# Optimization experiments

Measured on AMD Instinct MI355X. Metric: run time of the kernel, lower is better.

The kernel has to match this reference:

```python
import jax, jax.numpy as jnp
import numpy as np

NQ = 6       # total qubits
NF = 4
NL = 2       # layers
B = 65536    # batch
WEIGHT_INIT_STD = 0.01


def _apply_1q(state, gate, w):
    """Apply a 2x2 gate (shared (2,2) or per-sample (B,2,2)) to qubit w.
    state: (B, 2,2,2,2,2,2) complex64, axis w+1 is qubit w (PennyLane wire order)."""
    ax = w + 1
    s = jnp.moveaxis(state, ax, -1)
    shp = s.shape
    s = s.reshape(shp[0], -1, 2)
    if gate.ndim == 2:
        s = jnp.einsum('ij,bkj->bki', gate, s)
    else:
        s = jnp.einsum('bij,bkj->bki', gate, s)
    return jnp.moveaxis(s.reshape(shp), -1, ax)


def _cnot(state, c, t):
    """CNOT with control c, target t: flip target axis where control bit = 1."""
    ac, at = c + 1, t + 1
    s0 = jax.lax.index_in_dim(state, 0, ac, keepdims=True)
    s1 = jnp.flip(jax.lax.index_in_dim(state, 1, ac, keepdims=True), axis=at)
    return jnp.concatenate([s0, s1], axis=ac)


def _ry(theta):
    ct = jnp.cos(theta * 0.5)
    st = jnp.sin(theta * 0.5)
    return jnp.stack([jnp.stack([ct, -st]), jnp.stack([st, ct])]).astype(jnp.complex64)


def _circuit(x, weights, ancilla_bias):
    b = x.shape[0]
    state = jnp.zeros((b,) + (2,) * NQ, jnp.complex64)
    state = state.at[(slice(None),) + (0,) * NQ].set(1.0)  # |000000>
    # RX(x[:, w]) encoding on qubits 0..3 (batched gates)
    half = x.astype(jnp.float32) * 0.5
    c = jnp.cos(half).astype(jnp.complex64)
    s = (-1j) * jnp.sin(half).astype(jnp.complex64)
    for w in range(NF):
        g = jnp.stack([jnp.stack([c[:, w], s[:, w]], -1),
                       jnp.stack([s[:, w], c[:, w]], -1)], -2)  # (B,2,2)
        state = _apply_1q(state, g, w)
    # RY ancilla init on qubits 4, 5
    state = _apply_1q(state, _ry(ancilla_bias[0]), 4)
    state = _apply_1q(state, _ry(ancilla_bias[1]), 5)
    # entangling layers: CNOT ring then RY rotations
    for l in range(weights.shape[0]):
        for w in range(NQ):
            state = _cnot(state, w, (w + 1) % NQ)
        for w in range(NQ):
            state = _apply_1q(state, _ry(weights[l, w]), w)
    # <Z_w> for w in 0..3
    p = state.real ** 2 + state.imag ** 2  # (B,2,...,2)
    outs = []
    for w in range(NF):
        pw = p.sum(axis=tuple(a for a in range(1, NQ + 1) if a != w + 1))  # (B,2)
        outs.append(pw[:, 0] - pw[:, 1])
    return jnp.stack(outs, -1).astype(jnp.float32)  # (B, 4)


def setup_inputs() -> dict:
    key = jax.random.key(0)
    k1, k2 = jax.random.split(key)
    x = jax.random.normal(k1, (B, NF), jnp.float32)
    weights = jax.random.normal(k2, (NL, NQ), jnp.float32) * WEIGHT_INIT_STD
    ancilla_bias = jnp.zeros((2,), jnp.float32)
    return {"x": x, "weights": weights, "ancilla_bias": ancilla_bias}


def reference(x, weights, ancilla_bias):
    return _circuit(x, weights, ancilla_bias)
```

## Files before the change

### kernel.cpp

```cpp
#include <hip/hip_runtime.h>


#define NL 2

typedef float v2f __attribute__((ext_vector_type(2)));

template<int CTRL>
__device__ __forceinline__ float dppf(float v) {
    return __int_as_float(__builtin_amdgcn_update_dpp(
        0, __float_as_int(v), CTRL, 0xF, 0xF, true));
}
template<int CTRL>
__device__ __forceinline__ v2f dpp2(v2f v) {
    v2f r; r.x = dppf<CTRL>(v.x); r.y = dppf<CTRL>(v.y); return r;
}
__device__ __forceinline__ v2f splat(float f) { v2f r; r.x = f; r.y = f; return r; }

#define QP_XOR1  0xB1
#define QP_XOR2  0x4E
#define QP_C45   0xB4
#define QP_BC0   0x00
#define QP_BC1   0x55
#define QP_BC2   0xAA
#define QP_BC3   0xFF

__global__ __launch_bounds__(256) void qcirc6_dpp_kernel(
    const float* __restrict__ x,
    const float* __restrict__ weights,
    const float* __restrict__ bias,
    float* __restrict__ out,
    int B)
{
    const int gid = blockIdx.x * blockDim.x + threadIdx.x;
    const int sample = gid >> 2;
    if (sample >= B) return;
    const int sub = gid & 3;

    float sh, ch;
    __sincosf(x[gid] * 0.5f, &sh, &ch);
    const float c0 = dppf<QP_BC0>(ch), s0 = dppf<QP_BC0>(sh);
    const float c1 = dppf<QP_BC1>(ch), s1 = dppf<QP_BC1>(sh);
    const float c2 = dppf<QP_BC2>(ch), s2 = dppf<QP_BC2>(sh);
    const float c3 = dppf<QP_BC3>(ch), s3 = dppf<QP_BC3>(sh);

    float sb0, cb0, sb1, cb1;
    __sincosf(bias[0] * 0.5f, &sb0, &cb0);
    __sincosf(bias[1] * 0.5f, &sb1, &cb1);
    const float laneF = ((sub & 2) ? sb0 : cb0) * ((sub & 1) ? sb1 : cb1);

    const float v01[4] = {c0 * c1, c0 * s1, s0 * c1, s0 * s1};
    const float v23[4] = {c2 * c3, c2 * s3, s2 * c3, s2 * s3};

    v2f a[16];
    #pragma unroll
    for (int t = 0; t < 16; ++t) {
        const float v = laneF * v01[t >> 2] * v23[t & 3];
        const int m = ((t & 1) + ((t >> 1) & 1) + ((t >> 2) & 1) + ((t >> 3) & 1)) & 3;
        v2f av;
        if      (m == 0) { av.x =  v;   av.y = 0.f; }
        else if (m == 1) { av.x = 0.f;  av.y = -v;  }
        else if (m == 2) { av.x = -v;   av.y = 0.f; }
        else             { av.x = 0.f;  av.y =  v;  }
        a[t] = av;
    }

    const bool c50 = (sub & 1) != 0;

    #pragma unroll
    for (int l = 0; l < NL; ++l) {
        #pragma unroll
        for (int pass = 0; pass < 3; ++pass) {
            const int cm = 8 >> pass, tm = 4 >> pass;
            #pragma unroll
            for (int t = 0; t < 16; ++t) {
                if ((t & cm) && !(t & tm)) {
                    const int j = t | tm;
                    v2f tmp = a[t]; a[t] = a[j]; a[j] = tmp;
                }
            }
        }
        #pragma unroll
        for (int t = 1; t < 16; t += 2) a[t] = dpp2<QP_XOR2>(a[t]);
        #pragma unroll
        for (int t = 0; t < 16; ++t) a[t] = dpp2<QP_C45>(a[t]);

        float st, ct;
        __sincosf(weights[l * 6 + 0] * 0.5f, &st, &ct);
        {
            const v2f al = splat(c50 ? -st : ct);
            const v2f be = splat(c50 ?  ct : -st);
            const v2f ga = splat(c50 ?  ct : st);
            const v2f de = splat(c50 ?  st : ct);
            #pragma unroll
            for (int t = 0; t < 8; ++t) {
                const int j = t | 8;
                const v2f a0 = a[t], a1 = a[j];
                a[t] = al * a0 + be * a1;
                a[j] = ga * a0 + de * a1;
            }
        }
        #pragma unroll
        for (int w = 1; w < 4; ++w) {
            __sincosf(weights[l * 6 + w] * 0.5f, &st, &ct);
            const v2f ctv = splat(ct), stv = splat(st);
            const int m = 8 >> w;
            #pragma unroll
            for (int t = 0; t < 16; ++t) {
                if (t & m) continue;
                const int j = t | m;
                const v2f a0 = a[t], a1 = a[j];
                a[t] = ctv * a0 - stv * a1;
                a[j] = stv * a0 + ctv * a1;
            }
        }
        __sincosf(weights[l * 6 + 4] * 0.5f, &st, &ct);
        {
            const v2f ctv = splat(ct), sgv = splat((sub & 2) ? st : -st);
            #pragma unroll
            for (int t = 0; t < 16; ++t) {
                const v2f p = dpp2<QP_XOR2>(a[t]);
                a[t] = ctv * a[t] + sgv * p;
            }
        }
        __sincosf(weights[l * 6 + 5] * 0.5f, &st, &ct);
        {
            const v2f ctv = splat(ct), sgv = splat((sub & 1) ? st : -st);
            #pragma unroll
            for (int t = 0; t < 16; ++t) {
                const v2f p = dpp2<QP_XOR1>(a[t]);
                a[t] = ctv * a[t] + sgv * p;
            }
        }
    }

    float z0 = 0.f, z1 = 0.f, z2 = 0.f, z3 = 0.f;
    #pragma unroll
    for (int t = 0; t < 16; ++t) {
        const v2f sq = a[t] * a[t];
        const float p = sq.x + sq.y;
        z0 += (t & 8) ? -p : p;
        z1 += (t & 4) ? -p : p;
        z2 += (t & 2) ? -p : p;
        z3 += (t & 1) ? -p : p;
    }
    z0 += dppf<QP_XOR1>(z0); z0 += dppf<QP_XOR2>(z0);
    z1 += dppf<QP_XOR1>(z1); z1 += dppf<QP_XOR2>(z1);
    z2 += dppf<QP_XOR1>(z2); z2 += dppf<QP_XOR2>(z2);
    z3 += dppf<QP_XOR1>(z3); z3 += dppf<QP_XOR2>(z3);

    const float zsel = (sub == 0) ? z0 : (sub == 1) ? z1 : (sub == 2) ? z2 : z3;
    out[gid] = zsel;
}

extern "C" void kernel_launch(void* const* d_in, const int* in_sizes, int n_in,
                              void* d_out, int out_size, void* d_ws, size_t ws_size,
                              hipStream_t stream) {
    const float* x       = (const float*)d_in[0];
    const float* weights = (const float*)d_in[1];
    const float* bias    = (const float*)d_in[2];
    float* out = (float*)d_out;
    const int B = in_sizes[0] / 4;
    const int threads = B * 4;
    qcirc6_dpp_kernel<<<(threads + 255) / 256, 256, 0, stream>>>(x, weights, bias, out, B);
}
```

Before: 62.97 us.

## Hold full 64-amplitude state per thread instead of splitting across four lanes

```diff
diff --git a/kernel.cpp b/kernel.cpp
--- a/kernel.cpp
+++ b/kernel.cpp
@@ -5,151 +5,114 @@
 
 typedef float v2f __attribute__((ext_vector_type(2)));
 
-template<int CTRL>
-__device__ __forceinline__ float dppf(float v) {
-    return __int_as_float(__builtin_amdgcn_update_dpp(
-        0, __float_as_int(v), CTRL, 0xF, 0xF, true));
-}
-template<int CTRL>
-__device__ __forceinline__ v2f dpp2(v2f v) {
-    v2f r; r.x = dppf<CTRL>(v.x); r.y = dppf<CTRL>(v.y); return r;
-}
-__device__ __forceinline__ v2f splat(float f) { v2f r; r.x = f; r.y = f; return r; }
-
-#define QP_XOR1  0xB1
-#define QP_XOR2  0x4E
-#define QP_C45   0xB4
-#define QP_BC0   0x00
-#define QP_BC1   0x55
-#define QP_BC2   0xAA
-#define QP_BC3   0xFF
-
-__global__ __launch_bounds__(256) void qcirc6_dpp_kernel(
+__global__ __launch_bounds__(256, 1) void qcirc6_reg_kernel(
     const float* __restrict__ x,
     const float* __restrict__ weights,
     const float* __restrict__ bias,
     float* __restrict__ out,
     int B)
 {
-    const int gid = blockIdx.x * blockDim.x + threadIdx.x;
-    const int sample = gid >> 2;
+    const int sample = blockIdx.x * blockDim.x + threadIdx.x;
     if (sample >= B) return;
-    const int sub = gid & 3;
 
-    float sh, ch;
-    __sincosf(x[gid] * 0.5f, &sh, &ch);
-    const float c0 = dppf<QP_BC0>(ch), s0 = dppf<QP_BC0>(sh);
-    const float c1 = dppf<QP_BC1>(ch), s1 = dppf<QP_BC1>(sh);
-    const float c2 = dppf<QP_BC2>(ch), s2 = dppf<QP_BC2>(sh);
-    const float c3 = dppf<QP_BC3>(ch), s3 = dppf<QP_BC3>(sh);
-
+    const float4 xv = *reinterpret_cast<const float4*>(x + sample * 4);
+    float s0, c0, s1, c1, s2, c2, s3, c3;
+    __sincosf(xv.x * 0.5f, &s0, &c0);
+    __sincosf(xv.y * 0.5f, &s1, &c1);
+    __sincosf(xv.z * 0.5f, &s2, &c2);
+    __sincosf(xv.w * 0.5f, &s3, &c3);
     float sb0, cb0, sb1, cb1;
     __sincosf(bias[0] * 0.5f, &sb0, &cb0);
     __sincosf(bias[1] * 0.5f, &sb1, &cb1);
-    const float laneF = ((sub & 2) ? sb0 : cb0) * ((sub & 1) ? sb1 : cb1);
 
     const float v01[4] = {c0 * c1, c0 * s1, s0 * c1, s0 * s1};
     const float v23[4] = {c2 * c3, c2 * s3, s2 * c3, s2 * s3};
+    const float v45[4] = {cb0 * cb1, cb0 * sb1, sb0 * cb1, sb0 * sb1};
 
-    v2f a[16];
+    v2f a[64];
     #pragma unroll
-    for (int t = 0; t < 16; ++t) {
-        const float v = laneF * v01[t >> 2] * v23[t & 3];
-        const int m = ((t & 1) + ((t >> 1) & 1) + ((t >> 2) & 1) + ((t >> 3) & 1)) & 3;
-        v2f av;
-        if      (m == 0) { av.x =  v;   av.y = 0.f; }
-        else if (m == 1) { av.x = 0.f;  av.y = -v;  }
-        else if (m == 2) { av.x = -v;   av.y = 0.f; }
-        else             { av.x = 0.f;  av.y =  v;  }
-        a[t] = av;
+    for (int h = 0; h < 16; ++h) {
+        const int m = ((h & 1) + ((h >> 1) & 1) + ((h >> 2) & 1) + ((h >> 3) & 1)) & 3;
+        const float vh = v01[h >> 2] * v23[h & 3];
+        #pragma unroll
+        for (int l = 0; l < 4; ++l) {
+            const float val = vh * v45[l];
+            v2f av;
+            if      (m == 0) { av.x =  val; av.y = 0.f;  }
+            else if (m == 1) { av.x = 0.f;  av.y = -val; }
+            else if (m == 2) { av.x = -val; av.y = 0.f;  }
+            else             { av.x = 0.f;  av.y =  val; }
+            a[(h << 2) | l] = av;
+        }
     }
 
-    const bool c50 = (sub & 1) != 0;
+    #define CNOT(CM, TM)                                              \
+        _Pragma("unroll")                                             \
+        for (int i = 0; i < 64; ++i) {                                \
+            if ((i & (CM)) && !(i & (TM))) {                          \
+                const int j = i | (TM);                               \
+                const v2f tmp = a[i]; a[i] = a[j]; a[j] = tmp;        \
+            }                                                         \
+        }
 
     #pragma unroll
     for (int l = 0; l < NL; ++l) {
+        CNOT(32, 16)
+        CNOT(16,  8)
+        CNOT( 8,  4)
+        CNOT( 4,  2)
+        CNOT( 2,  1)
+        CNOT( 1, 32)
+
         #pragma unroll
-        for (int pass = 0; pass < 3; ++pass) {
-            const int cm = 8 >> pass, tm = 4 >> pass;
+        for (int w = 0; w < 6; ++w) {
+            float st, ct;
+            __sincosf(weights[l * 6 + w] * 0.5f, &st, &ct);
+            v2f ctv; ctv.x = ct; ctv.y = ct;
+            v2f stv; stv.x = st; stv.y = st;
+            const int m = 32 >> w;
             #pragma unroll
-            for (int t = 0; t < 16; ++t) {
-                if ((t & cm) && !(t & tm)) {
-                    const int j = t | tm;
-                    v2f tmp = a[t]; a[t] = a[j]; a[j] = tmp;
-                }
-            }
-        }
-        #pragma unroll
-        for (int t = 1; t < 16; t += 2) a[t] = dpp2<QP_XOR2>(a[t]);
-        #pragma unroll
-        for (int t = 0; t < 16; ++t) a[t] = dpp2<QP_C45>(a[t]);
-
-        float st, ct;
-        __sincosf(weights[l * 6 + 0] * 0.5f, &st, &ct);
-        {
-            const v2f al = splat(c50 ? -st : ct);
-            const v2f be = splat(c50 ?  ct : -st);
-            const v2f ga = splat(c50 ?  ct : st);
-            const v2f de = splat(c50 ?  st : ct);
-            #pragma unroll
-            for (int t = 0; t < 8; ++t) {
-                const int j = t | 8;
-                const v2f a0 = a[t], a1 = a[j];
-                a[t] = al * a0 + be * a1;
-                a[j] = ga * a0 + de * a1;
-            }
-        }
-        #pragma unroll
-        for (int w = 1; w < 4; ++w) {
-            __sincosf(weights[l * 6 + w] * 0.5f, &st, &ct);
-            const v2f ctv = splat(ct), stv = splat(st);
-            const int m = 8 >> w;
-            #pragma unroll
-            for (int t = 0; t < 16; ++t) {
-                if (t & m) continue;
-                const int j = t | m;
-                const v2f a0 = a[t], a1 = a[j];
-                a[t] = ctv * a0 - stv * a1;
+            for (int i = 0; i < 64; ++i) {
+                if (i & m) continue;
+                const int j = i | m;
+                const v2f a0 = a[i], a1 = a[j];
+                a[i] = ctv * a0 - stv * a1;
                 a[j] = stv * a0 + ctv * a1;
             }
         }
-        __sincosf(weights[l * 6 + 4] * 0.5f, &st, &ct);
-        {
-            const v2f ctv = splat(ct), sgv = splat((sub & 2) ? st : -st);
-            #pragma unroll
-            for (int t = 0; t < 16; ++t) {
-                const v2f p = dpp2<QP_XOR2>(a[t]);
-                a[t] = ctv * a[t] + sgv * p;
-            }
-        }
-        __sincosf(weights[l * 6 + 5] * 0.5f, &st, &ct);
-        {
-            const v2f ctv = splat(ct), sgv = splat((sub & 1) ? st : -st);
-            #pragma unroll
-            for (int t = 0; t < 16; ++t) {
-                const v2f p = dpp2<QP_XOR1>(a[t]);
-                a[t] = ctv * a[t] + sgv * p;
-            }
-        }
     }
+    #undef CNOT
 
-    float z0 = 0.f, z1 = 0.f, z2 = 0.f, z3 = 0.f;
+    v2f s16[16];
     #pragma unroll
-    for (int t = 0; t < 16; ++t) {
-        const v2f sq = a[t] * a[t];
-        const float p = sq.x + sq.y;
-        z0 += (t & 8) ? -p : p;
-        z1 += (t & 4) ? -p : p;
-        z2 += (t & 2) ? -p : p;
-        z3 += (t & 1) ? -p : p;
+    for (int h = 0; h < 16; ++h) {
+        const v2f p0 = a[4 * h + 0] * a[4 * h + 0];
+        const v2f p1 = a[4 * h + 1] * a[4 * h + 1];
+        const v2f p2 = a[4 * h + 2] * a[4 * h + 2];
+        const v2f p3 = a[4 * h + 3] * a[4 * h + 3];
+        s16[h] = (p0 + p1) + (p2 + p3);
     }
-    z0 += dppf<QP_XOR1>(z0); z0 += dppf<QP_XOR2>(z0);
-    z1 += dppf<QP_XOR1>(z1); z1 += dppf<QP_XOR2>(z1);
-    z2 += dppf<QP_XOR1>(z2); z2 += dppf<QP_XOR2>(z2);
-    z3 += dppf<QP_XOR1>(z3); z3 += dppf<QP_XOR2>(z3);
+    v2f u8[8], z3v; z3v.x = 0.f; z3v.y = 0.f;
+    #pragma unroll
+    for (int h = 0; h < 8; ++h) {
+        u8[h] = s16[2 * h] + s16[2 * h + 1];
+        z3v  += s16[2 * h] - s16[2 * h + 1];
+    }
+    v2f u4[4], z2v; z2v.x = 0.f; z2v.y = 0.f;
+    #pragma unroll
+    for (int h = 0; h < 4; ++h) {
+        u4[h] = u8[2 * h] + u8[2 * h + 1];
+        z2v  += u8[2 * h] - u8[2 * h + 1];
+    }
+    const v2f z1v = (u4[0] - u4[1]) + (u4[2] - u4[3]);
+    const v2f z0v = (u4[0] + u4[1]) - (u4[2] + u4[3]);
 
-    const float zsel = (sub == 0) ? z0 : (sub == 1) ? z1 : (sub == 2) ? z2 : z3;
-    out[gid] = zsel;
+    float4 o;
+    o.x = z0v.x + z0v.y;
+    o.y = z1v.x + z1v.y;
+    o.z = z2v.x + z2v.y;
+    o.w = z3v.x + z3v.y;
+    *reinterpret_cast<float4*>(out + sample * 4) = o;
 }
 
 extern "C" void kernel_launch(void* const* d_in, const int* in_sizes, int n_in,
@@ -160,6 +123,5 @@
     const float* bias    = (const float*)d_in[2];
     float* out = (float*)d_out;
     const int B = in_sizes[0] / 4;
-    const int threads = B * 4;
-    qcirc6_dpp_kernel<<<(threads + 255) / 256, 256, 0, stream>>>(x, weights, bias, out, B);
+    qcirc6_reg_kernel<<<(B + 255) / 256, 256, 0, stream>>>(x, weights, bias, out, B);
 }
```

Result: faster. 60.98 us (-3.2%).
